# Kernel tuning notes

Measured on AMD Instinct MI355X. Metric: run time of the kernel, lower is better.

Reference implementation:

```python
import jax, jax.numpy as jnp
import numpy as np

N = 100000
E = 1600000
IN_CH = 128
HID = 64
OUT = 16
L = 5
G = 512
BN_EPS = 1e-5


def setup_inputs() -> dict:
    key = jax.random.key(0)
    ks = jax.random.split(key, 24)
    x = jax.random.normal(ks[0], (N, IN_CH), dtype=jnp.float32)
    edge_index = jax.random.randint(ks[1], (2, E), 0, N, dtype=jnp.int32)
    batch = jnp.sort(jax.random.randint(ks[2], (N,), 0, G, dtype=jnp.int32))
    s = 0.05
    inp = {
        'x': x,
        'edge_index': edge_index,
        'batch': batch,
        'eps': jnp.zeros((L,), jnp.float32),
        'W1_0': jax.random.normal(ks[3], (IN_CH, HID), jnp.float32) * s,
        'b1_0': jnp.zeros((HID,), jnp.float32),
        'W1_r': jax.random.normal(ks[4], (L - 1, HID, HID), jnp.float32) * s,
        'b1_r': jnp.zeros((L - 1, HID), jnp.float32),
        'g_a': jnp.ones((L, HID), jnp.float32),
        'be_a': jnp.zeros((L, HID), jnp.float32),
        'm_a': jax.random.normal(ks[5], (L, HID), jnp.float32) * 0.1,
        'v_a': jax.random.uniform(ks[6], (L, HID), jnp.float32, 0.5, 1.5),
        'W2': jax.random.normal(ks[7], (L, HID, HID), jnp.float32) * s,
        'b2': jnp.zeros((L, HID), jnp.float32),
        'g_b': jnp.ones((L, HID), jnp.float32),
        'be_b': jnp.zeros((L, HID), jnp.float32),
        'm_b': jax.random.normal(ks[8], (L, HID), jnp.float32) * 0.1,
        'v_b': jax.random.uniform(ks[9], (L, HID), jnp.float32, 0.5, 1.5),
        'Wc': jax.random.normal(ks[10], (HID * L, OUT), jnp.float32) * s,
        'bc': jnp.zeros((OUT,), jnp.float32),
    }
    return inp


def _bn(h, gamma, beta, mean, var):
    # inference-mode BatchNorm1d
    return (h - mean) * (gamma * jax.lax.rsqrt(var + BN_EPS)) + beta


def reference(x, edge_index, batch, eps, W1_0, b1_0, W1_r, b1_r,
              g_a, be_a, m_a, v_a, W2, b2, g_b, be_b, m_b, v_b, Wc, bc):
    src, dst = edge_index[0], edge_index[1]
    h = x
    readouts = []
    for l in range(L):
        # GIN aggregation: sum of neighbor features via gather + scatter_add
        agg = jax.ops.segment_sum(h[src], dst, num_segments=N)
        z = (1.0 + eps[l]) * h + agg
        # MLP: Linear -> BN -> ReLU -> Linear
        W1 = W1_0 if l == 0 else W1_r[l - 1]
        b1 = b1_0 if l == 0 else b1_r[l - 1]
        z = z @ W1 + b1
        z = jax.nn.relu(_bn(z, g_a[l], be_a[l], m_a[l], v_a[l]))
        z = z @ W2[l] + b2[l]
        # outer BN + ReLU (dropout is identity in eval mode)
        h = jax.nn.relu(_bn(z, g_b[l], be_b[l], m_b[l], v_b[l]))
        # graph-level sum pooling
        readouts.append(jax.ops.segment_sum(h, batch, num_segments=G))
    graph_repr = jnp.concatenate(readouts, axis=-1)  # [G, HID*L]
    return graph_repr @ Wc + bc
```

## Files before the change

kernel.cpp:

```cpp
#include <hip/hip_runtime.h>

#define NN 100000
#define EE 1600000
#define GG 512
#define LL 5
#define HID 64
#define RCOLS (HID*LL)
#define OUTC 16
#define NGRP ((NN + 63) / 64)
#define NBUCK ((NN + 255) / 256)
#define BCAP 4864

typedef unsigned int uint;
typedef unsigned short ushort;
typedef __attribute__((ext_vector_type(8))) short short8;
typedef __attribute__((ext_vector_type(4))) float f32x4;

__device__ __forceinline__ float bf2f(ushort u) {
    return __uint_as_float(((uint)u) << 16);
}
__device__ __forceinline__ ushort f2bf(float f) {
    uint u = __float_as_uint(f);
    u = (u + 0x7fffu + ((u >> 16) & 1u)) >> 16;
    return (ushort)u;
}
__device__ __forceinline__ uint pack2(float a, float b) {
    return (uint)f2bf(a) | ((uint)f2bf(b) << 16);
}
__device__ __forceinline__ float lo16(uint p) { return __uint_as_float(p << 16); }
__device__ __forceinline__ float hi16(uint p) { return __uint_as_float(p & 0xffff0000u); }

__global__ __launch_bounds__(256) void init_bcur_kernel(int* __restrict__ bcur)
{
    int i = blockIdx.x * 256 + threadIdx.x;
    if (i < NBUCK) bcur[i] = i * BCAP;
}

__global__ __launch_bounds__(256) void binfill_kernel(
    const int* __restrict__ src, const int* __restrict__ dst,
    int* __restrict__ bcur, uint* __restrict__ bin)
{
    __shared__ int hcnt[NBUCK], hbase[NBUCK];
    const int tid = threadIdx.x;
    for (int b = tid; b < NBUCK; b += 256) hcnt[b] = 0;
    __syncthreads();
    const int chunk = (EE + gridDim.x - 1) / gridDim.x;
    const int e0 = blockIdx.x * chunk;
    const int e1 = (e0 + chunk < EE) ? e0 + chunk : EE;
    for (int e = e0 + tid; e < e1; e += 256)
        atomicAdd(&hcnt[dst[e] >> 8], 1);
    __syncthreads();
    for (int b = tid; b < NBUCK; b += 256) {
        int c = hcnt[b];
        hbase[b] = c ? atomicAdd(&bcur[b], c) : 0;
        hcnt[b] = 0;
    }
    __syncthreads();
    for (int e = e0 + tid; e < e1; e += 256) {
        int d = dst[e];
        int b = d >> 8;
        int off = atomicAdd(&hcnt[b], 1);
        bin[hbase[b] + off] = ((uint)src[e] << 8) | (uint)(d & 255);
    }
}

__global__ __launch_bounds__(256) void bucket_csr_kernel(
    const uint* __restrict__ bin, const int* __restrict__ bcur,
    int* __restrict__ rowptr, int* __restrict__ rowend, int* __restrict__ col)
{
    __shared__ int h[256], s[256];
    const int b = blockIdx.x;
    const int tid = threadIdx.x;
    const int base = b * BCAP;
    const int cnt = bcur[b] - base;
    h[tid] = 0;
    __syncthreads();
    for (int i = tid; i < cnt; i += 256)
        atomicAdd(&h[bin[base + i] & 255], 1);
    __syncthreads();
    const int own = h[tid];
    s[tid] = own;
    __syncthreads();
    int val = own;
    for (int off = 1; off < 256; off <<= 1) {
        int other = (tid >= off) ? s[tid - off] : 0;
        __syncthreads();
        val += other;
        s[tid] = val;
        __syncthreads();
    }
    const int excl = val - own;
    const int node = b * 256 + tid;
    if (node < NN) {
        rowptr[node] = base + excl;
        rowend[node] = base + excl + own;
    }
    h[tid] = base + excl;
    __syncthreads();
    for (int i = tid; i < cnt; i += 256) {
        uint w = bin[base + i];
        int p = atomicAdd(&h[w & 255], 1);
        col[p] = (int)(w >> 8);
    }
}

__global__ __launch_bounds__(256) void prep_w_kernel(
    const float* __restrict__ W2, const float* __restrict__ W1_r,
    ushort* __restrict__ w2t, ushort* __restrict__ w1nt)
{
    const int i = blockIdx.x * 256 + threadIdx.x;
    if (i < 5 * 4096) {
        int l = i >> 12, r = i & 4095, k = r >> 6, c = r & 63;
        w2t[l * 4608 + c * 72 + k] = f2bf(W2[l * 4096 + k * 64 + c]);
    }
    if (i < 4 * 4096) {
        int l = i >> 12, r = i & 4095, k = r >> 6, c = r & 63;
        w1nt[l * 4608 + c * 72 + k] = f2bf(W1_r[l * 4096 + k * 64 + c]);
    }
}

__global__ __launch_bounds__(256) void ingemm_kernel(
    const float* __restrict__ x, const float* __restrict__ W1,
    ushort* __restrict__ Y0)
{
    __shared__ __align__(16) ushort W1t[64 * 136];
    __shared__ __align__(16) ushort zA[4][16 * 72];

    for (int e = threadIdx.x; e < 64 * 128; e += 256) {
        int c = e & 63, k = e >> 6;
        W1t[c * 136 + k] = f2bf(W1[k * 64 + c]);
    }
    __syncthreads();

    const int lane = threadIdx.x & 63;
    const int wave = threadIdx.x >> 6;
    const int fr = lane & 15, fq = lane >> 4;
    ushort* zw = zA[wave];

    for (int grp = blockIdx.x; grp < NGRP; grp += gridDim.x) {
        const int base = grp * 64 + wave * 16;
        if (base >= NN) continue;

        short8 az[4];
        #pragma unroll
        for (int h = 0; h < 4; ++h) {
            const float* xp = x + (size_t)(base + fr) * 128 + h * 32 + fq * 8;
            float4 f0 = *(const float4*)xp;
            float4 f1 = *(const float4*)(xp + 4);
            short8 a;
            a[0] = (short)f2bf(f0.x); a[1] = (short)f2bf(f0.y);
            a[2] = (short)f2bf(f0.z); a[3] = (short)f2bf(f0.w);
            a[4] = (short)f2bf(f1.x); a[5] = (short)f2bf(f1.y);
            a[6] = (short)f2bf(f1.z); a[7] = (short)f2bf(f1.w);
            az[h] = a;
        }
        #pragma unroll
        for (int t = 0; t < 4; ++t) {
            f32x4 acc = {0.f, 0.f, 0.f, 0.f};
            #pragma unroll
            for (int h = 0; h < 4; ++h) {
                short8 bw = *(const short8*)&W1t[(t * 16 + fr) * 136 + h * 32 + fq * 8];
                acc = __builtin_amdgcn_mfma_f32_16x16x32_bf16(az[h], bw, acc, 0, 0, 0);
            }
            #pragma unroll
            for (int r = 0; r < 4; ++r)
                zw[(fq * 4 + r) * 72 + t * 16 + fr] = f2bf(acc[r]);
        }
        #pragma unroll 4
        for (int i = 0; i < 16; ++i)
            Y0[(size_t)(base + i) * 64 + lane] = zw[i * 72 + lane];
    }
}

template<bool LAST>
__global__ __launch_bounds__(256, 7) void gin_layer_kernel(
    const ushort* __restrict__ Y,
    const int* __restrict__ rowptr, const int* __restrict__ rowend,
    const int* __restrict__ col,
    const float* __restrict__ eps_arr, int l,
    const float* __restrict__ b1,
    const ushort* __restrict__ w2t,
    const float* __restrict__ b2,
    const float* __restrict__ g_a, const float* __restrict__ be_a,
    const float* __restrict__ m_a, const float* __restrict__ v_a,
    const float* __restrict__ g_b, const float* __restrict__ be_b,
    const float* __restrict__ m_b, const float* __restrict__ v_b,
    const ushort* __restrict__ w1nt,
    const int* __restrict__ batch,
    ushort* __restrict__ Ynext,
    float* __restrict__ readout,
    int layer_off)
{
    __shared__ __align__(16) ushort zA[4][16 * 72];
    __shared__ float2 bnA[64], bnB[64];
    __shared__ __align__(16) int idxs[4][144];

    if (threadIdx.x < 64) {
        int c = threadIdx.x;
        float sa = g_a[c] * rsqrtf(v_a[c] + 1e-5f);
        float sb = g_b[c] * rsqrtf(v_b[c] + 1e-5f);
        bnA[c] = make_float2(sa, be_a[c] + (b1[c] - m_a[c]) * sa);
        bnB[c] = make_float2(sb, be_b[c] + (b2[c] - m_b[c]) * sb);
    }
    const float eps_l = 1.0f + eps_arr[l];
    __syncthreads();

    const int lane = threadIdx.x & 63;
    const int wave = threadIdx.x >> 6;
    const int fr = lane & 15, fq = lane >> 4;
    const int c4 = (lane & 15) * 4;
    const int sl = (lane >> 4) & 1;
    const int rb = (lane >> 5) * 72;
    ushort* zw = zA[wave];
    int* idw = idxs[wave];
    const float2 ba0 = bnA[c4], ba1 = bnA[c4 + 1], ba2 = bnA[c4 + 2], ba3 = bnA[c4 + 3];

    for (int grp = blockIdx.x; grp < NGRP; grp += gridDim.x) {
        const int base = grp * 64 + wave * 16;
        if (base >= NN) continue;

        for (int i = 0; i < 16; i += 2) {
            const int rowA = base + i, rowB = base + i + 1;
            int ja = rowptr[rowA];
            const int reA = rowend[rowA];
            int jb = reA;
            const int reB = rowend[rowB];
            float a0 = 0.f, a1 = 0.f, a2 = 0.f, a3 = 0.f;
            while (ja < reA || jb < reB) {
                int cntA = reA - ja; cntA = cntA > 64 ? 64 : cntA;
                int cntB = reB - jb; cntB = cntB > 64 ? 64 : cntB;
                {
                    int ia = ja + (lane < cntA ? lane : 0);
                    int ca = col[ia];
                    idw[lane] = (lane < cntA) ? ca : NN;
                    int ib = jb + (lane < cntB ? lane : 0);
                    int cb = col[ib];
                    idw[72 + lane] = (lane < cntB) ? cb : NN;
                    if (lane < 8) { idw[64 + lane] = NN; idw[136 + lane] = NN; }
                }
                const int niA = (cntA + 1) >> 1, niB = (cntB + 1) >> 1;
                const int ni = niA > niB ? niA : niB;
                for (int t = 0; t < ni; t += 4) {
                    int r0 = idw[rb + (t + 0) * 2 + sl];
                    int r1 = idw[rb + (t + 1) * 2 + sl];
                    int r2 = idw[rb + (t + 2) * 2 + sl];
                    int r3 = idw[rb + (t + 3) * 2 + sl];
                    uint2 w0 = *(const uint2*)&Y[(size_t)r0 * 64 + c4];
                    uint2 w1 = *(const uint2*)&Y[(size_t)r1 * 64 + c4];
                    uint2 w2 = *(const uint2*)&Y[(size_t)r2 * 64 + c4];
                    uint2 w3 = *(const uint2*)&Y[(size_t)r3 * 64 + c4];
                    a0 += (lo16(w0.x) + lo16(w1.x)) + (lo16(w2.x) + lo16(w3.x));
                    a1 += (hi16(w0.x) + hi16(w1.x)) + (hi16(w2.x) + hi16(w3.x));
                    a2 += (lo16(w0.y) + lo16(w1.y)) + (lo16(w2.y) + lo16(w3.y));
                    a3 += (hi16(w0.y) + hi16(w1.y)) + (hi16(w2.y) + hi16(w3.y));
                }
                ja += cntA; jb += cntB;
            }
            a0 += __shfl_xor(a0, 16); a1 += __shfl_xor(a1, 16);
            a2 += __shfl_xor(a2, 16); a3 += __shfl_xor(a3, 16);
            const int myrow = (lane < 32) ? rowA : rowB;
            uint2 wr = *(const uint2*)&Y[(size_t)myrow * 64 + c4];
            a0 += eps_l * lo16(wr.x); a1 += eps_l * hi16(wr.x);
            a2 += eps_l * lo16(wr.y); a3 += eps_l * hi16(wr.y);
            float z0 = fmaxf(a0 * ba0.x + ba0.y, 0.f);
            float z1 = fmaxf(a1 * ba1.x + ba1.y, 0.f);
            float z2 = fmaxf(a2 * ba2.x + ba2.y, 0.f);
            float z3 = fmaxf(a3 * ba3.x + ba3.y, 0.f);
            if ((lane & 31) < 16) {
                uint2 pz;
                pz.x = pack2(z0, z1);
                pz.y = pack2(z2, z3);
                *(uint2*)&zw[(i + (lane >> 5)) * 72 + c4] = pz;
            }
        }

        short8 a2f[2];
        a2f[0] = *(const short8*)&zw[fr * 72 + fq * 8];
        a2f[1] = *(const short8*)&zw[fr * 72 + 32 + fq * 8];
        #pragma unroll
        for (int t = 0; t < 4; ++t) {
            f32x4 acc = {0.f, 0.f, 0.f, 0.f};
            short8 bw0 = *(const short8*)&w2t[(t * 16 + fr) * 72 + fq * 8];
            short8 bw1 = *(const short8*)&w2t[(t * 16 + fr) * 72 + 32 + fq * 8];
            acc = __builtin_amdgcn_mfma_f32_16x16x32_bf16(a2f[0], bw0, acc, 0, 0, 0);
            acc = __builtin_amdgcn_mfma_f32_16x16x32_bf16(a2f[1], bw1, acc, 0, 0, 0);
            float2 bn = bnB[t * 16 + fr];
            #pragma unroll
            for (int r = 0; r < 4; ++r) {
                float v = fmaxf(acc[r] * bn.x + bn.y, 0.f);
                zw[(fq * 4 + r) * 72 + t * 16 + fr] = f2bf(v);
            }
        }

        {
            int curg = batch[base];
            float racc = 0.f;
            #pragma unroll 4
            for (int i = 0; i < 16; ++i) {
                const float v = bf2f(zw[i * 72 + lane]);
                const int g = batch[base + i];
                if (g != curg) {
                    unsafeAtomicAdd(readout + (size_t)curg * RCOLS + layer_off + lane, racc);
                    curg = g;
                    racc = v;
                } else {
                    racc += v;
                }
            }
            unsafeAtomicAdd(readout + (size_t)curg * RCOLS + layer_off + lane, racc);
        }

        if constexpr (!LAST) {
            short8 a3f[2];
            a3f[0] = *(const short8*)&zw[fr * 72 + fq * 8];
            a3f[1] = *(const short8*)&zw[fr * 72 + 32 + fq * 8];
            #pragma unroll
            for (int t = 0; t < 4; ++t) {
                f32x4 acc = {0.f, 0.f, 0.f, 0.f};
                short8 bw0 = *(const short8*)&w1nt[(t * 16 + fr) * 72 + fq * 8];
                short8 bw1 = *(const short8*)&w1nt[(t * 16 + fr) * 72 + 32 + fq * 8];
                acc = __builtin_amdgcn_mfma_f32_16x16x32_bf16(a3f[0], bw0, acc, 0, 0, 0);
                acc = __builtin_amdgcn_mfma_f32_16x16x32_bf16(a3f[1], bw1, acc, 0, 0, 0);
                #pragma unroll
                for (int r = 0; r < 4; ++r)
                    zw[(fq * 4 + r) * 72 + t * 16 + fr] = f2bf(acc[r]);
            }
            #pragma unroll 4
            for (int i = 0; i < 16; ++i)
                Ynext[(size_t)(base + i) * 64 + lane] = zw[i * 72 + lane];
        }
    }
}

__global__ __launch_bounds__(256) void final_gemm(
    const float* __restrict__ R, const float* __restrict__ Wc,
    const float* __restrict__ bc, float* __restrict__ out)
{
    const int tid = blockIdx.x * 256 + threadIdx.x;
    if (tid >= GG * OUTC) return;
    const int g = tid >> 4;
    const int o = tid & 15;
    float acc = bc[o];
    const float* r = R + (size_t)g * RCOLS;
    #pragma unroll 8
    for (int k = 0; k < RCOLS; ++k)
        acc += r[k] * Wc[k * OUTC + o];
    out[tid] = acc;
}

extern "C" void kernel_launch(void* const* d_in, const int* in_sizes, int n_in,
                              void* d_out, int out_size, void* d_ws, size_t ws_size,
                              hipStream_t stream)
{
    const float* x    = (const float*)d_in[0];
    const int*   ei   = (const int*)d_in[1];
    const int*   batch= (const int*)d_in[2];
    const float* eps  = (const float*)d_in[3];
    const float* W1_0 = (const float*)d_in[4];
    const float* b1_0 = (const float*)d_in[5];
    const float* W1_r = (const float*)d_in[6];
    const float* b1_r = (const float*)d_in[7];
    const float* g_a  = (const float*)d_in[8];
    const float* be_a = (const float*)d_in[9];
    const float* m_a  = (const float*)d_in[10];
    const float* v_a  = (const float*)d_in[11];
    const float* W2   = (const float*)d_in[12];
    const float* b2   = (const float*)d_in[13];
    const float* g_b  = (const float*)d_in[14];
    const float* be_b = (const float*)d_in[15];
    const float* m_b  = (const float*)d_in[16];
    const float* v_b  = (const float*)d_in[17];
    const float* Wc   = (const float*)d_in[18];
    const float* bc   = (const float*)d_in[19];
    float* out = (float*)d_out;

    const int* src = ei;
    const int* dst = ei + EE;

    char* ws = (char*)d_ws;
    int*    rowptr  = (int*)(ws);
    int*    rowend  = (int*)(ws + 524288);
    int*    bcur    = (int*)(ws + 1048576);
    int*    col     = (int*)(ws + 1572864);
    uint*   bin     = (uint*)(ws + 9437184);
    ushort* y_a     = (ushort*)(ws + 17301504);
    ushort* y_b     = (ushort*)(ws + 30212096);
    float*  readout = (float*)(ws + 43122688);
    ushort* w2t_g   = (ushort*)(ws + 43778048);
    ushort* w1nt_g  = (ushort*)(ws + 43824128);

    hipMemsetAsync(readout, 0, (size_t)GG * RCOLS * 4, stream);
    hipMemsetAsync(y_a + (size_t)NN * 64, 0, 128, stream);
    hipMemsetAsync(y_b + (size_t)NN * 64, 0, 128, stream);

    init_bcur_kernel<<<(NBUCK + 255) / 256, 256, 0, stream>>>(bcur);
    prep_w_kernel<<<80, 256, 0, stream>>>(W2, W1_r, w2t_g, w1nt_g);
    ingemm_kernel<<<NGRP, 256, 0, stream>>>(x, W1_0, y_a);
    binfill_kernel<<<256, 256, 0, stream>>>(src, dst, bcur, bin);
    bucket_csr_kernel<<<NBUCK, 256, 0, stream>>>(bin, bcur, rowptr, rowend, col);

    ushort* y_cur = y_a;
    ushort* y_nxt = y_b;

    for (int l = 0; l < LL; ++l) {
        const float* b1 = (l == 0) ? b1_0 : (b1_r + (size_t)(l - 1) * 64);
        const int off = l * 64;
        const ushort* w2t  = w2t_g + (size_t)l * 4608;
        const ushort* w1nt = (l < LL - 1) ? (w1nt_g + (size_t)l * 4608) : w1nt_g;
        if (l < LL - 1) {
            gin_layer_kernel<false><<<NGRP, 256, 0, stream>>>(
                y_cur, rowptr, rowend, col, eps, l, b1,
                w2t, b2 + off,
                g_a + off, be_a + off, m_a + off, v_a + off,
                g_b + off, be_b + off, m_b + off, v_b + off,
                w1nt, batch, y_nxt, readout, off);
        } else {
            gin_layer_kernel<true><<<NGRP, 256, 0, stream>>>(
                y_cur, rowptr, rowend, col, eps, l, b1,
                w2t, b2 + off,
                g_a + off, be_a + off, m_a + off, v_a + off,
                g_b + off, be_b + off, m_b + off, v_b + off,
                w1nt, batch, y_nxt, readout, off);
        }
        ushort* t = y_cur; y_cur = y_nxt; y_nxt = t;
    }

    final_gemm<<<(GG * OUTC + 255) / 256, 256, 0, stream>>>(readout, Wc, bc, out);
}
```

Baseline: 312.7 us.

## Split CSR rows into source-range segments to improve gather cache locality

The CSR build now sorts each node's neighbours into four source-index ranges and stores per-node segment offsets as an int4. The aggregation loop walks all 16 rows of a wave one segment at a time, keeping 32 accumulators live, so concurrent gathers touch a narrower slice of the feature matrix and hit cache more often. In exchange it runs more loop iterations, with many only partly filled (about four edges per segment instead of about sixteen per row), issues more index loads, and raises register pressure, so occupancy is lowered from 7 to 6. The workspace layout is also repacked, with the edge bin buffer sharing space with one feature buffer.

```diff
diff --git a/kernel.cpp b/kernel.cpp
--- a/kernel.cpp
+++ b/kernel.cpp
@@ -10,6 +10,7 @@
 #define NGRP ((NN + 63) / 64)
 #define NBUCK ((NN + 255) / 256)
 #define BCAP 4864
+#define SEGSZ 25600
 
 typedef unsigned int uint;
 typedef unsigned short ushort;
@@ -66,19 +67,25 @@
 
 __global__ __launch_bounds__(256) void bucket_csr_kernel(
     const uint* __restrict__ bin, const int* __restrict__ bcur,
-    int* __restrict__ rowptr, int* __restrict__ rowend, int* __restrict__ col)
-{
-    __shared__ int h[256], s[256];
+    int4* __restrict__ rowseg4, int* __restrict__ rowend, int* __restrict__ col)
+{
+    __shared__ int h4[256][4];
+    __shared__ int s[256];
+    __shared__ int c4[256][4];
     const int b = blockIdx.x;
     const int tid = threadIdx.x;
     const int base = b * BCAP;
     const int cnt = bcur[b] - base;
-    h[tid] = 0;
-    __syncthreads();
-    for (int i = tid; i < cnt; i += 256)
-        atomicAdd(&h[bin[base + i] & 255], 1);
-    __syncthreads();
-    const int own = h[tid];
+    h4[tid][0] = 0; h4[tid][1] = 0; h4[tid][2] = 0; h4[tid][3] = 0;
+    __syncthreads();
+    for (int i = tid; i < cnt; i += 256) {
+        uint w = bin[base + i];
+        int srcv = (int)(w >> 8);
+        atomicAdd(&h4[w & 255][srcv / SEGSZ], 1);
+    }
+    __syncthreads();
+    const int t0 = h4[tid][0], t1 = h4[tid][1], t2 = h4[tid][2], t3 = h4[tid][3];
+    const int own = t0 + t1 + t2 + t3;
     s[tid] = own;
     __syncthreads();
     int val = own;
@@ -89,18 +96,19 @@
         s[tid] = val;
         __syncthreads();
     }
-    const int excl = val - own;
+    const int nb = base + (val - own);
     const int node = b * 256 + tid;
     if (node < NN) {
-        rowptr[node] = base + excl;
-        rowend[node] = base + excl + own;
-    }
-    h[tid] = base + excl;
+        rowseg4[node] = make_int4(nb, nb + t0, nb + t0 + t1, nb + t0 + t1 + t2);
+        rowend[node] = nb + own;
+    }
+    c4[tid][0] = nb; c4[tid][1] = nb + t0; c4[tid][2] = nb + t0 + t1; c4[tid][3] = nb + t0 + t1 + t2;
     __syncthreads();
     for (int i = tid; i < cnt; i += 256) {
         uint w = bin[base + i];
-        int p = atomicAdd(&h[w & 255], 1);
-        col[p] = (int)(w >> 8);
+        int srcv = (int)(w >> 8);
+        int p = atomicAdd(&c4[w & 255][srcv / SEGSZ], 1);
+        col[p] = srcv;
     }
 }
 
@@ -173,9 +181,9 @@
 }
 
 template<bool LAST>
-__global__ __launch_bounds__(256, 7) void gin_layer_kernel(
+__global__ __launch_bounds__(256, 6) void gin_layer_kernel(
     const ushort* __restrict__ Y,
-    const int* __restrict__ rowptr, const int* __restrict__ rowend,
+    const int4* __restrict__ rowseg4, const int* __restrict__ rowend,
     const int* __restrict__ col,
     const float* __restrict__ eps_arr, int l,
     const float* __restrict__ b1,
@@ -208,58 +216,75 @@
     const int lane = threadIdx.x & 63;
     const int wave = threadIdx.x >> 6;
     const int fr = lane & 15, fq = lane >> 4;
-    const int c4 = (lane & 15) * 4;
+    const int c4c = (lane & 15) * 4;
     const int sl = (lane >> 4) & 1;
     const int rb = (lane >> 5) * 72;
     ushort* zw = zA[wave];
     int* idw = idxs[wave];
-    const float2 ba0 = bnA[c4], ba1 = bnA[c4 + 1], ba2 = bnA[c4 + 2], ba3 = bnA[c4 + 3];
+    const float2 ba0 = bnA[c4c], ba1 = bnA[c4c + 1], ba2 = bnA[c4c + 2], ba3 = bnA[c4c + 3];
 
     for (int grp = blockIdx.x; grp < NGRP; grp += gridDim.x) {
         const int base = grp * 64 + wave * 16;
         if (base >= NN) continue;
 
-        for (int i = 0; i < 16; i += 2) {
-            const int rowA = base + i, rowB = base + i + 1;
-            int ja = rowptr[rowA];
-            const int reA = rowend[rowA];
-            int jb = reA;
-            const int reB = rowend[rowB];
-            float a0 = 0.f, a1 = 0.f, a2 = 0.f, a3 = 0.f;
-            while (ja < reA || jb < reB) {
-                int cntA = reA - ja; cntA = cntA > 64 ? 64 : cntA;
-                int cntB = reB - jb; cntB = cntB > 64 ? 64 : cntB;
-                {
-                    int ia = ja + (lane < cntA ? lane : 0);
-                    int ca = col[ia];
-                    idw[lane] = (lane < cntA) ? ca : NN;
-                    int ib = jb + (lane < cntB ? lane : 0);
-                    int cb = col[ib];
-                    idw[72 + lane] = (lane < cntB) ? cb : NN;
-                    if (lane < 8) { idw[64 + lane] = NN; idw[136 + lane] = NN; }
+        float ac[8][4];
+        #pragma unroll
+        for (int p = 0; p < 8; ++p) { ac[p][0] = 0.f; ac[p][1] = 0.f; ac[p][2] = 0.f; ac[p][3] = 0.f; }
+
+        for (int s = 0; s < 4; ++s) {
+            #pragma unroll
+            for (int p = 0; p < 8; ++p) {
+                const int rowA = base + 2 * p, rowB = rowA + 1;
+                int4 rA = rowseg4[rowA];
+                int4 rBv = rowseg4[rowB];
+                int eA = rowend[rowA];
+                int eB = rowend[rowB];
+                int ja  = s == 0 ? rA.x  : s == 1 ? rA.y  : s == 2 ? rA.z  : rA.w;
+                int reA = s == 0 ? rA.y  : s == 1 ? rA.z  : s == 2 ? rA.w  : eA;
+                int jb  = s == 0 ? rBv.x : s == 1 ? rBv.y : s == 2 ? rBv.z : rBv.w;
+                int reB = s == 0 ? rBv.y : s == 1 ? rBv.z : s == 2 ? rBv.w : eB;
+                while (ja < reA || jb < reB) {
+                    int cntA = reA - ja; cntA = cntA > 64 ? 64 : cntA;
+                    int cntB = reB - jb; cntB = cntB > 64 ? 64 : cntB;
+                    {
+                        int ia = ja + (lane < cntA ? lane : 0);
+                        int ca = col[ia];
+                        idw[lane] = (lane < cntA) ? ca : NN;
+                        int ib = jb + (lane < cntB ? lane : 0);
+                        int cb = col[ib];
+                        idw[72 + lane] = (lane < cntB) ? cb : NN;
+                        if (lane < 8) { idw[64 + lane] = NN; idw[136 + lane] = NN; }
+                    }
+                    const int niA = (cntA + 1) >> 1, niB = (cntB + 1) >> 1;
+                    const int ni = niA > niB ? niA : niB;
+                    for (int t = 0; t < ni; t += 4) {
+                        int r0 = idw[rb + (t + 0) * 2 + sl];
+                        int r1 = idw[rb + (t + 1) * 2 + sl];
+                        int r2 = idw[rb + (t + 2) * 2 + sl];
+                        int r3 = idw[rb + (t + 3) * 2 + sl];
+                        uint2 w0 = *(const uint2*)&Y[(size_t)r0 * 64 + c4c];
+                        uint2 w1 = *(const uint2*)&Y[(size_t)r1 * 64 + c4c];
+                        uint2 w2 = *(const uint2*)&Y[(size_t)r2 * 64 + c4c];
+                        uint2 w3 = *(const uint2*)&Y[(size_t)r3 * 64 + c4c];
+                        ac[p][0] += (lo16(w0.x) + lo16(w1.x)) + (lo16(w2.x) + lo16(w3.x));
+                        ac[p][1] += (hi16(w0.x) + hi16(w1.x)) + (hi16(w2.x) + hi16(w3.x));
+                        ac[p][2] += (lo16(w0.y) + lo16(w1.y)) + (lo16(w2.y) + lo16(w3.y));
+                        ac[p][3] += (hi16(w0.y) + hi16(w1.y)) + (hi16(w2.y) + hi16(w3.y));
+                    }
+                    ja += cntA; jb += cntB;
                 }
-                const int niA = (cntA + 1) >> 1, niB = (cntB + 1) >> 1;
-                const int ni = niA > niB ? niA : niB;
-                for (int t = 0; t < ni; t += 4) {
-                    int r0 = idw[rb + (t + 0) * 2 + sl];
-                    int r1 = idw[rb + (t + 1) * 2 + sl];
-                    int r2 = idw[rb + (t + 2) * 2 + sl];
-                    int r3 = idw[rb + (t + 3) * 2 + sl];
-                    uint2 w0 = *(const uint2*)&Y[(size_t)r0 * 64 + c4];
-                    uint2 w1 = *(const uint2*)&Y[(size_t)r1 * 64 + c4];
-                    uint2 w2 = *(const uint2*)&Y[(size_t)r2 * 64 + c4];
-                    uint2 w3 = *(const uint2*)&Y[(size_t)r3 * 64 + c4];
-                    a0 += (lo16(w0.x) + lo16(w1.x)) + (lo16(w2.x) + lo16(w3.x));
-                    a1 += (hi16(w0.x) + hi16(w1.x)) + (hi16(w2.x) + hi16(w3.x));
-                    a2 += (lo16(w0.y) + lo16(w1.y)) + (lo16(w2.y) + lo16(w3.y));
-                    a3 += (hi16(w0.y) + hi16(w1.y)) + (hi16(w2.y) + hi16(w3.y));
-                }
-                ja += cntA; jb += cntB;
-            }
+            }
+        }
+
+        #pragma unroll
+        for (int p = 0; p < 8; ++p) {
+            const int i = 2 * p;
+            const int rowA = base + i, rowB = rowA + 1;
+            float a0 = ac[p][0], a1 = ac[p][1], a2 = ac[p][2], a3 = ac[p][3];
             a0 += __shfl_xor(a0, 16); a1 += __shfl_xor(a1, 16);
             a2 += __shfl_xor(a2, 16); a3 += __shfl_xor(a3, 16);
             const int myrow = (lane < 32) ? rowA : rowB;
-            uint2 wr = *(const uint2*)&Y[(size_t)myrow * 64 + c4];
+            uint2 wr = *(const uint2*)&Y[(size_t)myrow * 64 + c4c];
             a0 += eps_l * lo16(wr.x); a1 += eps_l * hi16(wr.x);
             a2 += eps_l * lo16(wr.y); a3 += eps_l * hi16(wr.y);
             float z0 = fmaxf(a0 * ba0.x + ba0.y, 0.f);
@@ -270,7 +295,7 @@
                 uint2 pz;
                 pz.x = pack2(z0, z1);
                 pz.y = pack2(z2, z3);
-                *(uint2*)&zw[(i + (lane >> 5)) * 72 + c4] = pz;
+                *(uint2*)&zw[(i + (lane >> 5)) * 72 + c4c] = pz;
             }
         }
 
@@ -378,16 +403,16 @@
     const int* dst = ei + EE;
 
     char* ws = (char*)d_ws;
-    int*    rowptr  = (int*)(ws);
-    int*    rowend  = (int*)(ws + 524288);
-    int*    bcur    = (int*)(ws + 1048576);
-    int*    col     = (int*)(ws + 1572864);
-    uint*   bin     = (uint*)(ws + 9437184);
-    ushort* y_a     = (ushort*)(ws + 17301504);
-    ushort* y_b     = (ushort*)(ws + 30212096);
-    float*  readout = (float*)(ws + 43122688);
-    ushort* w2t_g   = (ushort*)(ws + 43778048);
-    ushort* w1nt_g  = (ushort*)(ws + 43824128);
+    int4*   rowseg4 = (int4*)(ws);
+    int*    rowend  = (int*)(ws + 1638400);
+    int*    bcur    = (int*)(ws + 2097152);
+    int*    col     = (int*)(ws + 2621440);
+    uint*   bin     = (uint*)(ws + 10485760);
+    ushort* y_b     = (ushort*)(ws + 10485760);
+    ushort* y_a     = (ushort*)(ws + 23592960);
+    float*  readout = (float*)(ws + 36700160);
+    ushort* w2t_g   = (ushort*)(ws + 37748736);
+    ushort* w1nt_g  = (ushort*)(ws + 37812224);
 
     hipMemsetAsync(readout, 0, (size_t)GG * RCOLS * 4, stream);
     hipMemsetAsync(y_a + (size_t)NN * 64, 0, 128, stream);
@@ -397,7 +422,7 @@
     prep_w_kernel<<<80, 256, 0, stream>>>(W2, W1_r, w2t_g, w1nt_g);
     ingemm_kernel<<<NGRP, 256, 0, stream>>>(x, W1_0, y_a);
     binfill_kernel<<<256, 256, 0, stream>>>(src, dst, bcur, bin);
-    bucket_csr_kernel<<<NBUCK, 256, 0, stream>>>(bin, bcur, rowptr, rowend, col);
+    bucket_csr_kernel<<<NBUCK, 256, 0, stream>>>(bin, bcur, rowseg4, rowend, col);
 
     ushort* y_cur = y_a;
     ushort* y_nxt = y_b;
@@ -409,14 +434,14 @@
         const ushort* w1nt = (l < LL - 1) ? (w1nt_g + (size_t)l * 4608) : w1nt_g;
         if (l < LL - 1) {
             gin_layer_kernel<false><<<NGRP, 256, 0, stream>>>(
-                y_cur, rowptr, rowend, col, eps, l, b1,
+                y_cur, rowseg4, rowend, col, eps, l, b1,
                 w2t, b2 + off,
                 g_a + off, be_a + off, m_a + off, v_a + off,
                 g_b + off, be_b + off, m_b + off, v_b + off,
                 w1nt, batch, y_nxt, readout, off);
         } else {
             gin_layer_kernel<true><<<NGRP, 256, 0, stream>>>(
-                y_cur, rowptr, rowend, col, eps, l, b1,
+                y_cur, rowseg4, rowend, col, eps, l, b1,
                 w2t, b2 + off,
                 g_a + off, be_a + off, m_a + off, v_a + off,
                 g_b + off, be_b + off, m_b + off, v_b + off,
```

After: 1.086 ms. +247.3%, slower.
